# Optimization experiments

Measured on AMD Instinct MI355X. Metric: run time of the kernel, lower is better.

The kernel has to match this reference:

```python
import jax, jax.numpy as jnp
import numpy as np

R = 32          # voxel resolution
K = 3           # conv3d kernel size
GROUPS = 8      # GroupNorm groups
EPS_GN = 1e-5

def swish(x):
    return x * jax.nn.sigmoid(x)

def groupnorm(x, w, b):
    # x: (B, C, ...) -> normalize over (C//G, spatial) per group
    B, C = x.shape[0], x.shape[1]
    xs = x.reshape(B, GROUPS, C // GROUPS, -1)
    mu = xs.mean(axis=(2, 3), keepdims=True)
    var = xs.var(axis=(2, 3), keepdims=True)
    xs = (xs - mu) * jax.lax.rsqrt(var + EPS_GN)
    xs = xs.reshape(x.shape)
    shp = (1, C) + (1,) * (x.ndim - 2)
    return xs * w.reshape(shp) + b.reshape(shp)

def conv3d_same(x, w, b):
    y = jax.lax.conv_general_dilated(
        x, w, window_strides=(1, 1, 1), padding='SAME',
        dimension_numbers=('NCDHW', 'OIDHW', 'NCDHW'))
    return y + b[None, :, None, None, None]

def voxelize_coords(coords):
    # coords: (B,3,N) -> normalized coords in [0, R-1]
    nc = coords - coords.mean(axis=2, keepdims=True)
    scale = jnp.max(jnp.linalg.norm(nc, axis=1, keepdims=True), axis=2, keepdims=True) * 2.0
    nc = nc / scale + 0.5
    nc = jnp.clip(nc * R, 0.0, R - 1)
    return nc

def avg_voxelize(features, vox_coords):
    # features: (B,C,N), vox_coords: (B,3,N) int32 in [0,R-1]
    B, C, N = features.shape
    r3 = R * R * R
    flat = (vox_coords[:, 0] * R + vox_coords[:, 1]) * R + vox_coords[:, 2]  # (B,N)
    seg = (flat + jnp.arange(B, dtype=jnp.int32)[:, None] * r3).reshape(-1)
    feats = features.transpose(0, 2, 1).reshape(B * N, C)
    sums = jax.ops.segment_sum(feats, seg, num_segments=B * r3)
    cnt = jax.ops.segment_sum(jnp.ones((B * N,), features.dtype), seg, num_segments=B * r3)
    avg = sums / jnp.maximum(cnt, 1.0)[:, None]
    return avg.reshape(B, r3, C).transpose(0, 2, 1).reshape(B, C, R, R, R)

def trilinear_devoxelize(grid, nc):
    # grid: (B,C,R,R,R), nc: (B,3,N) float in [0,R-1]
    B, C = grid.shape[0], grid.shape[1]
    N = nc.shape[2]
    f = jnp.floor(nc)
    c0 = jnp.clip(f.astype(jnp.int32), 0, R - 1)
    c1 = jnp.clip(c0 + 1, 0, R - 1)
    w1 = nc - f
    w0 = 1.0 - w1
    gflat = grid.reshape(B, C, R * R * R)
    out = jnp.zeros((B, C, N), grid.dtype)
    for dx in (0, 1):
        for dy in (0, 1):
            for dz in (0, 1):
                xi = c1[:, 0] if dx else c0[:, 0]
                yi = c1[:, 1] if dy else c0[:, 1]
                zi = c1[:, 2] if dz else c0[:, 2]
                wx = w1[:, 0] if dx else w0[:, 0]
                wy = w1[:, 1] if dy else w0[:, 1]
                wz = w1[:, 2] if dz else w0[:, 2]
                idx = (xi * R + yi) * R + zi            # (B,N)
                vals = jnp.take_along_axis(gflat, idx[:, None, :], axis=2)
                out = out + vals * (wx * wy * wz)[:, None, :]
    return out

def setup_inputs() -> dict:
    key = jax.random.key(0)
    ks = jax.random.split(key, 16)
    B, Cin, Cout, N = 8, 64, 64, 16384
    s3 = 1.0 / np.sqrt(Cin * K * K * K)
    s3b = 1.0 / np.sqrt(Cout * K * K * K)
    s1 = 1.0 / np.sqrt(Cin)
    return {
        'features': jax.random.normal(ks[0], (B, Cin, N), jnp.float32),
        'coords': jax.random.normal(ks[1], (B, 3, N), jnp.float32),
        'conv1_w': jax.random.uniform(ks[2], (Cout, Cin, K, K, K), jnp.float32, -s3, s3),
        'conv1_b': jax.random.uniform(ks[3], (Cout,), jnp.float32, -s3, s3),
        'gn1_w': jnp.ones((Cout,), jnp.float32),
        'gn1_b': jnp.zeros((Cout,), jnp.float32),
        'conv2_w': jax.random.uniform(ks[4], (Cout, Cout, K, K, K), jnp.float32, -s3b, s3b),
        'conv2_b': jax.random.uniform(ks[5], (Cout,), jnp.float32, -s3b, s3b),
        'gn2_w': jnp.ones((Cout,), jnp.float32),
        'gn2_b': jnp.zeros((Cout,), jnp.float32),
        'pf_w': jax.random.uniform(ks[6], (Cout, Cin), jnp.float32, -s1, s1),
        'pf_b': jax.random.uniform(ks[7], (Cout,), jnp.float32, -s1, s1),
        'pf_gn_w': jnp.ones((Cout,), jnp.float32),
        'pf_gn_b': jnp.zeros((Cout,), jnp.float32),
    }

def reference(features, coords, conv1_w, conv1_b, gn1_w, gn1_b,
              conv2_w, conv2_b, gn2_w, gn2_b, pf_w, pf_b, pf_gn_w, pf_gn_b):
    coords_d = jax.lax.stop_gradient(coords)
    nc = voxelize_coords(coords_d)                       # (B,3,N) in [0,R-1]
    vox = jnp.round(nc).astype(jnp.int32)
    grid = avg_voxelize(features, vox)                   # (B,C,R,R,R)
    # voxel conv stack (dropout = identity in eval)
    g = conv3d_same(grid, conv1_w, conv1_b)
    g = swish(groupnorm(g, gn1_w, gn1_b))
    g = conv3d_same(g, conv2_w, conv2_b)
    g = groupnorm(g, gn2_w, gn2_b)
    voxel_feats = trilinear_devoxelize(g, nc)            # (B,Cout,N)
    # point branch: 1x1 conv1d + GroupNorm + Swish
    p = jnp.einsum('oc,bcn->bon', pf_w, features) + pf_b[None, :, None]
    p = swish(groupnorm(p, pf_gn_w, pf_gn_b))
    return voxel_feats + p
```

## Files before the change

### kernel.cpp

```cpp
#include <hip/hip_runtime.h>
#include <hip/hip_bf16.h>
#include <stdint.h>

#define PB 8
#define PN 16384
#define PC 64
#define PR 32
#define PR3 32768
#define PRP 34

typedef __attribute__((ext_vector_type(8))) short bf16x8;
typedef __attribute__((ext_vector_type(16))) float f32x16;

__device__ __forceinline__ unsigned short f2bf(float f) {
  union { float f; unsigned u; } v; v.f = f;
  unsigned r = v.u + 0x7FFFu + ((v.u >> 16) & 1u);
  return (unsigned short)(r >> 16);
}

__global__ void coord_stats_kernel(const float* __restrict__ coords, float* __restrict__ ms) {
  int b = blockIdx.x, t = threadIdx.x;
  __shared__ float wsum[4][3];
  __shared__ float wmax[4];
  __shared__ float meanv[3];
  const float* c0 = coords + (size_t)b * 3 * PN;
  float s0 = 0.f, s1 = 0.f, s2 = 0.f;
  for (int n = t; n < PN; n += 256) {
    s0 += c0[n]; s1 += c0[PN + n]; s2 += c0[2 * PN + n];
  }
  for (int off = 32; off > 0; off >>= 1) {
    s0 += __shfl_down(s0, off); s1 += __shfl_down(s1, off); s2 += __shfl_down(s2, off);
  }
  if ((t & 63) == 0) { wsum[t >> 6][0] = s0; wsum[t >> 6][1] = s1; wsum[t >> 6][2] = s2; }
  __syncthreads();
  if (t == 0) {
    for (int d = 0; d < 3; ++d)
      meanv[d] = (wsum[0][d] + wsum[1][d] + wsum[2][d] + wsum[3][d]) * (1.0f / PN);
  }
  __syncthreads();
  float m0 = meanv[0], m1 = meanv[1], m2 = meanv[2];
  float mx = 0.f;
  for (int n = t; n < PN; n += 256) {
    float dx = c0[n] - m0, dy = c0[PN + n] - m1, dz = c0[2 * PN + n] - m2;
    mx = fmaxf(mx, dx * dx + dy * dy + dz * dz);
  }
  for (int off = 32; off > 0; off >>= 1) mx = fmaxf(mx, __shfl_down(mx, off));
  if ((t & 63) == 0) wmax[t >> 6] = mx;
  __syncthreads();
  if (t == 0) {
    float m = fmaxf(fmaxf(wmax[0], wmax[1]), fmaxf(wmax[2], wmax[3]));
    ms[b * 4 + 0] = meanv[0]; ms[b * 4 + 1] = meanv[1]; ms[b * 4 + 2] = meanv[2];
    ms[b * 4 + 3] = 2.0f * sqrtf(m);
  }
}

__global__ void nc_vox_kernel(const float* __restrict__ coords, const float* __restrict__ ms,
                              float* __restrict__ nc, int* __restrict__ vflat) {
  int i = blockIdx.x * 256 + threadIdx.x;
  if (i >= PB * PN) return;
  int b = i >> 14, n = i & (PN - 1);
  float sc = ms[b * 4 + 3];
  int vi[3];
  #pragma unroll
  for (int d = 0; d < 3; ++d) {
    float c = coords[((size_t)b * 3 + d) * PN + n];
    float q = (c - ms[b * 4 + d]) / sc + 0.5f;
    float v = fminf(fmaxf(q * 32.0f, 0.0f), 31.0f);
    nc[((size_t)b * 3 + d) * PN + n] = v;
    vi[d] = (int)rintf(v);
  }
  vflat[i] = (vi[0] * PR + vi[1]) * PR + vi[2];
}

__global__ void scatter_kernel(const float* __restrict__ feats, const int* __restrict__ vflat,
                               float* __restrict__ sums, float* __restrict__ cnts) {
  int b = blockIdx.y, p0 = blockIdx.x * 64, t = threadIdx.x;
  __shared__ float fl[64 * 65];
  for (int k = 0; k < 16; ++k) {
    int i = t + k * 256;
    int c = i >> 6, p = i & 63;
    fl[c * 65 + p] = feats[((size_t)b * PC + c) * PN + p0 + p];
  }
  __syncthreads();
  if (t < 64) atomicAdd(&cnts[b * PR3 + vflat[b * PN + p0 + t]], 1.0f);
  int cc = t & 63, pp = t >> 6;
  for (int i = 0; i < 16; ++i) {
    int p = pp * 16 + i;
    int v = vflat[b * PN + p0 + p];
    atomicAdd(&sums[((size_t)b * PR3 + v) * PC + cc], fl[cc * 65 + p]);
  }
}

__global__ void finalize_kernel(const float* __restrict__ sums, const float* __restrict__ cnts,
                                unsigned short* __restrict__ g0) {
  int idx = blockIdx.x * 256 + threadIdx.x;
  int co = idx & 7, v = (idx >> 3) & (PR3 - 1), b = idx >> 18;
  float cnt = cnts[b * PR3 + v];
  float inv = 1.0f / fmaxf(cnt, 1.0f);
  const float4* sp = (const float4*)(sums + ((size_t)(b * PR3 + v) * PC) + co * 8);
  float4 A = sp[0], B4 = sp[1];
  float vals[8] = {A.x, A.y, A.z, A.w, B4.x, B4.y, B4.z, B4.w};
  unsigned short h[8];
  #pragma unroll
  for (int k = 0; k < 8; ++k) h[k] = f2bf(vals[k] * inv);
  int z = v >> 10, y = (v >> 5) & 31, x = v & 31;
  size_t o = ((((size_t)b * PRP + (z + 1)) * PRP + (y + 1)) * PRP + (x + 1)) * PC + co * 8;
  uint4 pk;
  pk.x = h[0] | ((unsigned)h[1] << 16); pk.y = h[2] | ((unsigned)h[3] << 16);
  pk.z = h[4] | ((unsigned)h[5] << 16); pk.w = h[6] | ((unsigned)h[7] << 16);
  *(uint4*)(g0 + o) = pk;
}

__global__ void tconv_kernel(const float* __restrict__ w, unsigned short* __restrict__ wkt) {
  int idx = blockIdx.x * 256 + threadIdx.x;
  if (idx >= 27 * 64 * 64) return;
  int i = idx & 63, o = (idx >> 6) & 63, tap = idx >> 12;
  wkt[idx] = f2bf(w[(o * 64 + i) * 27 + tap]);
}
__global__ void tpf_kernel(const float* __restrict__ pw, float* __restrict__ wt) {
  int idx = blockIdx.x * 256 + threadIdx.x;
  if (idx >= 4096) return;
  int o = idx & 63, ci = idx >> 6;
  wt[ci * 64 + o] = pw[o * 64 + ci];
}

__global__ __launch_bounds__(256, 1) void conv3_kernel(
    const unsigned short* __restrict__ gin, const unsigned short* __restrict__ wkt,
    const float* __restrict__ bias, float* __restrict__ outp, float* __restrict__ stats) {
  extern __shared__ char smem[];
  const int t = threadIdx.x;
  const int tile = blockIdx.x, b = blockIdx.y;
  const int tz = tile >> 4, ty = (tile >> 2) & 3, tx = tile & 3;
  const int z0 = tz * 8, y0 = ty * 8, x0 = tx * 8;

  {
    const size_t gbase = (size_t)b * (PRP * PRP * PRP * PC);
    for (int it = 0; it < 32; ++it) {
      int q = t + it * 256;
      if (q < 8000) {
        int vl = q >> 3, cc = q & 7;
        int zz = vl / 100, rem = vl - zz * 100;
        int yy = rem / 10, xx = rem - yy * 10;
        size_t go = gbase + (((size_t)(z0 + zz) * PRP + (y0 + yy)) * PRP + (x0 + xx)) * PC + cc * 8;
        uint4 d = *(const uint4*)(gin + go);
        *(uint4*)(smem + (vl * 128 + ((cc ^ (vl & 7)) << 4))) = d;
      }
    }
  }
  {
    #pragma unroll
    for (int u = 0; u < 2; ++u) {
      int q = t * 2 + u;
      int o = q >> 3, cc = q & 7;
      uint4 d = ((const uint4*)wkt)[q];
      *(uint4*)(smem + 128000 + (o * 128 + ((cc ^ (o & 7)) << 4))) = d;
    }
  }
  __syncthreads();

  const int wv = t >> 6, l31 = t & 31, hi = (t >> 5) & 1;
  int vbase[4];
  #pragma unroll
  for (int m = 0; m < 4; ++m) {
    int vi = wv * 128 + m * 32 + l31;
    int z = vi >> 6, y = (vi >> 3) & 7, x = vi & 7;
    vbase[m] = z * 100 + y * 10 + x;
  }

  f32x16 acc[4][2];
  #pragma unroll
  for (int m = 0; m < 4; ++m)
    #pragma unroll
    for (int nb = 0; nb < 2; ++nb)
      #pragma unroll
      for (int r = 0; r < 16; ++r) acc[m][nb][r] = 0.0f;

  for (int tap = 0; tap < 27; ++tap) {
    if (tap + 1 < 27) {
      char* wb = smem + 128000 + (((tap + 1) & 1) * 8192);
      #pragma unroll
      for (int u = 0; u < 2; ++u) {
        int q = t * 2 + u;
        int o = q >> 3, cc = q & 7;
        uint4 d = ((const uint4*)wkt)[(tap + 1) * 512 + q];
        *(uint4*)(wb + (o * 128 + ((cc ^ (o & 7)) << 4))) = d;
      }
    }
    const char* wb = smem + 128000 + ((tap & 1) * 8192);
    int dz = tap / 9, r9 = tap - dz * 9;
    int dy = r9 / 3, dx = r9 - dy * 3;
    int toff = dz * 100 + dy * 10 + dx;
    #pragma unroll
    for (int kk = 0; kk < 4; ++kk) {
      bf16x8 afr[4], bfr[2];
      #pragma unroll
      for (int m = 0; m < 4; ++m) {
        int vl = vbase[m] + toff;
        afr[m] = *(const bf16x8*)(smem + (vl * 128 + (((kk * 2 + hi) ^ (vl & 7)) << 4)));
      }
      #pragma unroll
      for (int nb = 0; nb < 2; ++nb) {
        int o = nb * 32 + l31;
        bfr[nb] = *(const bf16x8*)(wb + (o * 128 + (((kk * 2 + hi) ^ (o & 7)) << 4)));
      }
      #pragma unroll
      for (int m = 0; m < 4; ++m)
        #pragma unroll
        for (int nb = 0; nb < 2; ++nb)
          acc[m][nb] = __builtin_amdgcn_mfma_f32_32x32x16_bf16(afr[m], bfr[nb], acc[m][nb], 0, 0, 0);
    }
    __syncthreads();
  }

  float sg[2] = {0.f, 0.f}, ssg[2] = {0.f, 0.f};
  #pragma unroll
  for (int nb = 0; nb < 2; ++nb) {
    int cn = nb * 32 + l31;
    float bv = bias[cn];
    #pragma unroll
    for (int m = 0; m < 4; ++m) {
      #pragma unroll
      for (int r = 0; r < 16; ++r) {
        int row = (r & 3) + 8 * (r >> 2) + 4 * hi;
        int vi = wv * 128 + m * 32 + row;
        int Z = z0 + (vi >> 6), Y = y0 + ((vi >> 3) & 7), X = x0 + (vi & 7);
        int vg = (Z * PR + Y) * PR + X;
        float val = acc[m][nb][r] + bv;
        outp[((size_t)b * PR3 + vg) * PC + cn] = val;
        sg[nb] += val; ssg[nb] += val * val;
      }
    }
  }
  #pragma unroll
  for (int nb = 0; nb < 2; ++nb) {
    sg[nb] += __shfl_down(sg[nb], 32);
    ssg[nb] += __shfl_down(ssg[nb], 32);
    #pragma unroll
    for (int off = 1; off <= 4; off <<= 1) {
      sg[nb] += __shfl_xor(sg[nb], off);
      ssg[nb] += __shfl_xor(ssg[nb], off);
    }
  }
  if (hi == 0 && (l31 & 7) == 0) {
    #pragma unroll
    for (int nb = 0; nb < 2; ++nb) {
      int g = (nb * 32 + l31) >> 3;
      atomicAdd(&stats[((size_t)b * 8 + g) * 2 + 0], sg[nb]);
      atomicAdd(&stats[((size_t)b * 8 + g) * 2 + 1], ssg[nb]);
    }
  }
}

__global__ void gn_swish_bf16_kernel(const float* __restrict__ raw, const float* __restrict__ st,
                                     const float* __restrict__ gw, const float* __restrict__ gb,
                                     unsigned short* __restrict__ g1) {
  int idx = blockIdx.x * 256 + threadIdx.x;
  int co = idx & 7, v = (idx >> 3) & (PR3 - 1), b = idx >> 18;
  const float invM = 1.0f / (8.0f * PR3);
  float s = st[(b * 8 + co) * 2], ssv = st[(b * 8 + co) * 2 + 1];
  float mu = s * invM, var = ssv * invM - mu * mu;
  float rstd = rsqrtf(var + 1e-5f);
  const float4* rp = (const float4*)(raw + ((size_t)(b * PR3 + v) * PC + co * 8));
  float4 A = rp[0], B4 = rp[1];
  float vals[8] = {A.x, A.y, A.z, A.w, B4.x, B4.y, B4.z, B4.w};
  unsigned short h[8];
  #pragma unroll
  for (int k = 0; k < 8; ++k) {
    int c = co * 8 + k;
    float y = (vals[k] - mu) * rstd * gw[c] + gb[c];
    float sw = y / (1.0f + expf(-y));
    h[k] = f2bf(sw);
  }
  int z = v >> 10, yy = (v >> 5) & 31, x = v & 31;
  size_t o = ((((size_t)b * PRP + (z + 1)) * PRP + (yy + 1)) * PRP + (x + 1)) * PC + co * 8;
  uint4 pk;
  pk.x = h[0] | ((unsigned)h[1] << 16); pk.y = h[2] | ((unsigned)h[3] << 16);
  pk.z = h[4] | ((unsigned)h[5] << 16); pk.w = h[6] | ((unsigned)h[7] << 16);
  *(uint4*)(g1 + o) = pk;
}

__global__ void gn_inplace_kernel(float* __restrict__ raw, const float* __restrict__ st,
                                  const float* __restrict__ gw, const float* __restrict__ gb) {
  int idx = blockIdx.x * 256 + threadIdx.x;
  int co = idx & 7, v = (idx >> 3) & (PR3 - 1), b = idx >> 18;
  const float invM = 1.0f / (8.0f * PR3);
  float s = st[(b * 8 + co) * 2], ssv = st[(b * 8 + co) * 2 + 1];
  float mu = s * invM, var = ssv * invM - mu * mu;
  float rstd = rsqrtf(var + 1e-5f);
  float4* rp = (float4*)(raw + ((size_t)(b * PR3 + v) * PC + co * 8));
  float4 A = rp[0], B4 = rp[1];
  float vals[8] = {A.x, A.y, A.z, A.w, B4.x, B4.y, B4.z, B4.w};
  #pragma unroll
  for (int k = 0; k < 8; ++k) {
    int c = co * 8 + k;
    vals[k] = (vals[k] - mu) * rstd * gw[c] + gb[c];
  }
  rp[0] = make_float4(vals[0], vals[1], vals[2], vals[3]);
  rp[1] = make_float4(vals[4], vals[5], vals[6], vals[7]);
}

__global__ void pf_kernel(const float* __restrict__ feats, const float* __restrict__ wt,
                          const float* __restrict__ pb, float* __restrict__ praw,
                          float* __restrict__ stats) {
  int b = blockIdx.y, n0 = blockIdx.x * 64, t = threadIdx.x;
  __shared__ float fl[64 * 65];
  __shared__ float wl[64 * 64];
  for (int k = 0; k < 16; ++k) {
    int i = t + k * 256;
    int c = i >> 6, p = i & 63;
    fl[c * 65 + p] = feats[((size_t)b * PC + c) * PN + n0 + p];
    wl[i] = wt[i];
  }
  __syncthreads();
  int n = t & 63, q = t >> 6;
  float acc[16];
  #pragma unroll
  for (int j = 0; j < 16; ++j) acc[j] = pb[q * 16 + j];
  for (int ci = 0; ci < 64; ++ci) {
    float v = fl[ci * 65 + n];
    #pragma unroll
    for (int j = 0; j < 16; ++j) acc[j] += v * wl[ci * 64 + q * 16 + j];
  }
  float s[2] = {0.f, 0.f}, ss[2] = {0.f, 0.f};
  #pragma unroll
  for (int j = 0; j < 16; ++j) {
    int o = q * 16 + j;
    praw[((size_t)b * PC + o) * PN + n0 + n] = acc[j];
    int h = j >> 3;
    s[h] += acc[j]; ss[h] += acc[j] * acc[j];
  }
  #pragma unroll
  for (int h = 0; h < 2; ++h) {
    for (int off = 32; off > 0; off >>= 1) {
      s[h] += __shfl_down(s[h], off);
      ss[h] += __shfl_down(ss[h], off);
    }
  }
  if (n == 0) {
    #pragma unroll
    for (int h = 0; h < 2; ++h) {
      atomicAdd(&stats[((size_t)b * 8 + 2 * q + h) * 2 + 0], s[h]);
      atomicAdd(&stats[((size_t)b * 8 + 2 * q + h) * 2 + 1], ss[h]);
    }
  }
}

__global__ void devox_kernel(const float* __restrict__ g2, const float* __restrict__ nc,
                             const float* __restrict__ praw, const float* __restrict__ stpf,
                             const float* __restrict__ pgw, const float* __restrict__ pgb,
                             float* __restrict__ out) {
  int b = blockIdx.y, n0 = blockIdx.x * 64, t = threadIdx.x;
  __shared__ float lt[64][65];
  int wv = t >> 6, c = t & 63;
  for (int i = 0; i < 16; ++i) {
    int p = wv * 16 + i, n = n0 + p;
    float fx = nc[((size_t)b * 3 + 0) * PN + n];
    float fy = nc[((size_t)b * 3 + 1) * PN + n];
    float fz = nc[((size_t)b * 3 + 2) * PN + n];
    float flx = floorf(fx), fly = floorf(fy), flz = floorf(fz);
    int x0 = (int)flx, y0 = (int)fly, z0 = (int)flz;
    int x1 = min(x0 + 1, 31), y1 = min(y0 + 1, 31), z1 = min(z0 + 1, 31);
    float wx1 = fx - flx, wy1 = fy - fly, wz1 = fz - flz;
    float wx0 = 1.f - wx1, wy0 = 1.f - wy1, wz0 = 1.f - wz1;
    const float* gb2 = g2 + (size_t)b * PR3 * PC + c;
    float a = 0.f;
    a += gb2[(size_t)((x0 * PR + y0) * PR + z0) * PC] * (wx0 * wy0 * wz0);
    a += gb2[(size_t)((x0 * PR + y0) * PR + z1) * PC] * (wx0 * wy0 * wz1);
    a += gb2[(size_t)((x0 * PR + y1) * PR + z0) * PC] * (wx0 * wy1 * wz0);
    a += gb2[(size_t)((x0 * PR + y1) * PR + z1) * PC] * (wx0 * wy1 * wz1);
    a += gb2[(size_t)((x1 * PR + y0) * PR + z0) * PC] * (wx1 * wy0 * wz0);
    a += gb2[(size_t)((x1 * PR + y0) * PR + z1) * PC] * (wx1 * wy0 * wz1);
    a += gb2[(size_t)((x1 * PR + y1) * PR + z0) * PC] * (wx1 * wy1 * wz0);
    a += gb2[(size_t)((x1 * PR + y1) * PR + z1) * PC] * (wx1 * wy1 * wz1);
    lt[p][c] = a;
  }
  __syncthreads();
  int n = t & 63, q = t >> 6;
  const float invM = 1.0f / (8.0f * PN);
  float mu[2], rs[2];
  #pragma unroll
  for (int h = 0; h < 2; ++h) {
    float s = stpf[((size_t)b * 8 + 2 * q + h) * 2];
    float ssv = stpf[((size_t)b * 8 + 2 * q + h) * 2 + 1];
    float m_ = s * invM;
    mu[h] = m_;
    rs[h] = rsqrtf(ssv * invM - m_ * m_ + 1e-5f);
  }
  #pragma unroll
  for (int j = 0; j < 16; ++j) {
    int cc = q * 16 + j, h = j >> 3;
    float p_ = praw[((size_t)b * PC + cc) * PN + n0 + n];
    float y = (p_ - mu[h]) * rs[h] * pgw[cc] + pgb[cc];
    float sw = y / (1.0f + expf(-y));
    out[((size_t)b * PC + cc) * PN + n0 + n] = lt[n][cc] + sw;
  }
}

extern "C" void kernel_launch(void* const* d_in, const int* in_sizes, int n_in,
                              void* d_out, int out_size, void* d_ws, size_t ws_size,
                              hipStream_t stream) {
  (void)in_sizes; (void)n_in; (void)out_size; (void)ws_size;
  const float* features = (const float*)d_in[0];
  const float* coords   = (const float*)d_in[1];
  const float* conv1_w  = (const float*)d_in[2];
  const float* conv1_b  = (const float*)d_in[3];
  const float* gn1_w    = (const float*)d_in[4];
  const float* gn1_b    = (const float*)d_in[5];
  const float* conv2_w  = (const float*)d_in[6];
  const float* conv2_b  = (const float*)d_in[7];
  const float* gn2_w    = (const float*)d_in[8];
  const float* gn2_b    = (const float*)d_in[9];
  const float* pf_w     = (const float*)d_in[10];
  const float* pf_b     = (const float*)d_in[11];
  const float* pf_gn_w  = (const float*)d_in[12];
  const float* pf_gn_b  = (const float*)d_in[13];
  float* out = (float*)d_out;

  char* ws = (char*)d_ws;
  size_t off = 0;
  auto alloc = [&](size_t bytes) { size_t r = (off + 255) & ~(size_t)255; off = r + bytes; return r; };

  const size_t sz_nc   = (size_t)PB * 3 * PN * 4;
  const size_t sz_ms   = 256;
  const size_t sz_vf   = (size_t)PB * PN * 4;
  const size_t sz_cnt  = (size_t)PB * PR3 * 4;
  const size_t sz_st   = (size_t)PB * 8 * 2 * 4;
  const size_t sz_raw  = (size_t)PB * PR3 * PC * 4;
  const size_t sz_gpad = (size_t)PB * PRP * PRP * PRP * PC * 2;
  const size_t sz_wkt  = (size_t)27 * 64 * 64 * 2;
  const size_t sz_pfw  = (size_t)64 * 64 * 4;

  float*          nc    = (float*)(ws + alloc(sz_nc));
  float*          ms    = (float*)(ws + alloc(sz_ms));
  int*            vflat = (int*)(ws + alloc(sz_vf));
  float*          cnts  = (float*)(ws + alloc(sz_cnt));
  float*          st1   = (float*)(ws + alloc(sz_st));
  float*          st2   = (float*)(ws + alloc(sz_st));
  float*          stpf  = (float*)(ws + alloc(sz_st));
  float*          graw  = (float*)(ws + alloc(sz_raw));
  unsigned short* g0    = (unsigned short*)(ws + alloc(sz_gpad));
  unsigned short* g1    = (unsigned short*)(ws + alloc(sz_gpad));
  unsigned short* wkt1  = (unsigned short*)(ws + alloc(sz_wkt));
  unsigned short* wkt2  = (unsigned short*)(ws + alloc(sz_wkt));
  float*          pfwt  = (float*)(ws + alloc(sz_pfw));
  float*          praw  = (float*)g0;

  hipMemsetAsync(cnts, 0, sz_cnt, stream);
  hipMemsetAsync(graw, 0, sz_raw, stream);
  hipMemsetAsync(g0, 0, sz_gpad, stream);
  hipMemsetAsync(g1, 0, sz_gpad, stream);
  hipMemsetAsync(st1, 0, sz_st, stream);
  hipMemsetAsync(st2, 0, sz_st, stream);
  hipMemsetAsync(stpf, 0, sz_st, stream);

  tconv_kernel<<<(27 * 4096 + 255) / 256, 256, 0, stream>>>(conv1_w, wkt1);
  tconv_kernel<<<(27 * 4096 + 255) / 256, 256, 0, stream>>>(conv2_w, wkt2);
  tpf_kernel<<<16, 256, 0, stream>>>(pf_w, pfwt);

  coord_stats_kernel<<<PB, 256, 0, stream>>>(coords, ms);
  nc_vox_kernel<<<(PB * PN) / 256, 256, 0, stream>>>(coords, ms, nc, vflat);
  scatter_kernel<<<dim3(PN / 64, PB), 256, 0, stream>>>(features, vflat, graw, cnts);
  finalize_kernel<<<(PB * PR3 * 8) / 256, 256, 0, stream>>>(graw, cnts, g0);

  const size_t conv_lds = 128000 + 2 * 8192;
  conv3_kernel<<<dim3(64, PB), 256, conv_lds, stream>>>(g0, wkt1, conv1_b, graw, st1);
  gn_swish_bf16_kernel<<<(PB * PR3 * 8) / 256, 256, 0, stream>>>(graw, st1, gn1_w, gn1_b, g1);

  pf_kernel<<<dim3(PN / 64, PB), 256, 0, stream>>>(features, pfwt, pf_b, praw, stpf);

  conv3_kernel<<<dim3(64, PB), 256, conv_lds, stream>>>(g1, wkt2, conv2_b, graw, st2);
  gn_inplace_kernel<<<(PB * PR3 * 8) / 256, 256, 0, stream>>>(graw, st2, gn2_w, gn2_b);

  devox_kernel<<<dim3(PN / 64, PB), 256, 0, stream>>>(graw, nc, praw, stpf, pf_gn_w, pf_gn_b, out);
}
```

Baseline: 713.5 us.

## Fold second GroupNorm into devoxelize, zero only pad borders, register-tile pf

Removes the standalone in-place GroupNorm pass over the conv2 output. Instead, devox_kernel applies the per-channel scale and shift after trilinear interpolation, which is valid because the interpolation weights always sum to one. The full-buffer memsets of the padded bf16 grids are replaced by a kernel that zeroes only the border voxels, since the interior is overwritten anyway. The point-feature 1x1 conv is re-tiled so each thread computes a 4x4 block of outputs using float4 LDS loads and float4 stores, with a wave-level reduction for the statistics. Together these cut a large read/write pass over global memory and some memset traffic.

```diff
diff --git a/kernel.cpp b/kernel.cpp
--- a/kernel.cpp
+++ b/kernel.cpp
@@ -8,6 +8,7 @@
 #define PR 32
 #define PR3 32768
 #define PRP 34
+#define PRP3 (PRP * PRP * PRP)
 
 typedef __attribute__((ext_vector_type(8))) short bf16x8;
 typedef __attribute__((ext_vector_type(16))) float f32x16;
@@ -16,6 +17,16 @@
   union { float f; unsigned u; } v; v.f = f;
   unsigned r = v.u + 0x7FFFu + ((v.u >> 16) & 1u);
   return (unsigned short)(r >> 16);
+}
+
+__global__ void zero_pad_kernel(unsigned short* __restrict__ g) {
+  int idx = blockIdx.x * 256 + threadIdx.x;
+  if (idx >= PB * PRP3 * 8) return;
+  int v = (idx >> 3) % PRP3;
+  int z = v / (PRP * PRP), rem = v % (PRP * PRP), y = rem / PRP, x = rem % PRP;
+  bool border = (z == 0) | (z == PRP - 1) | (y == 0) | (y == PRP - 1) | (x == 0) | (x == PRP - 1);
+  if (!border) return;
+  *(uint4*)(g + ((size_t)idx << 3)) = make_uint4(0, 0, 0, 0);
 }
 
 __global__ void coord_stats_kernel(const float* __restrict__ coords, float* __restrict__ ms) {
@@ -279,79 +290,72 @@
   *(uint4*)(g1 + o) = pk;
 }
 
-__global__ void gn_inplace_kernel(float* __restrict__ raw, const float* __restrict__ st,
-                                  const float* __restrict__ gw, const float* __restrict__ gb) {
-  int idx = blockIdx.x * 256 + threadIdx.x;
-  int co = idx & 7, v = (idx >> 3) & (PR3 - 1), b = idx >> 18;
-  const float invM = 1.0f / (8.0f * PR3);
-  float s = st[(b * 8 + co) * 2], ssv = st[(b * 8 + co) * 2 + 1];
-  float mu = s * invM, var = ssv * invM - mu * mu;
-  float rstd = rsqrtf(var + 1e-5f);
-  float4* rp = (float4*)(raw + ((size_t)(b * PR3 + v) * PC + co * 8));
-  float4 A = rp[0], B4 = rp[1];
-  float vals[8] = {A.x, A.y, A.z, A.w, B4.x, B4.y, B4.z, B4.w};
-  #pragma unroll
-  for (int k = 0; k < 8; ++k) {
-    int c = co * 8 + k;
-    vals[k] = (vals[k] - mu) * rstd * gw[c] + gb[c];
-  }
-  rp[0] = make_float4(vals[0], vals[1], vals[2], vals[3]);
-  rp[1] = make_float4(vals[4], vals[5], vals[6], vals[7]);
-}
-
 __global__ void pf_kernel(const float* __restrict__ feats, const float* __restrict__ wt,
                           const float* __restrict__ pb, float* __restrict__ praw,
                           float* __restrict__ stats) {
   int b = blockIdx.y, n0 = blockIdx.x * 64, t = threadIdx.x;
-  __shared__ float fl[64 * 65];
+  __shared__ float fl[64 * 68];
   __shared__ float wl[64 * 64];
   for (int k = 0; k < 16; ++k) {
     int i = t + k * 256;
     int c = i >> 6, p = i & 63;
-    fl[c * 65 + p] = feats[((size_t)b * PC + c) * PN + n0 + p];
+    fl[c * 68 + p] = feats[((size_t)b * PC + c) * PN + n0 + p];
     wl[i] = wt[i];
   }
   __syncthreads();
-  int n = t & 63, q = t >> 6;
-  float acc[16];
-  #pragma unroll
-  for (int j = 0; j < 16; ++j) acc[j] = pb[q * 16 + j];
+  int po = (t & 15) * 4;
+  int oo = (t >> 4) * 4;
+  float acc[4][4];
+  #pragma unroll
+  for (int pi = 0; pi < 4; ++pi)
+    #pragma unroll
+    for (int oi = 0; oi < 4; ++oi) acc[pi][oi] = pb[oo + oi];
   for (int ci = 0; ci < 64; ++ci) {
-    float v = fl[ci * 65 + n];
-    #pragma unroll
-    for (int j = 0; j < 16; ++j) acc[j] += v * wl[ci * 64 + q * 16 + j];
-  }
-  float s[2] = {0.f, 0.f}, ss[2] = {0.f, 0.f};
-  #pragma unroll
-  for (int j = 0; j < 16; ++j) {
-    int o = q * 16 + j;
-    praw[((size_t)b * PC + o) * PN + n0 + n] = acc[j];
-    int h = j >> 3;
-    s[h] += acc[j]; ss[h] += acc[j] * acc[j];
-  }
-  #pragma unroll
-  for (int h = 0; h < 2; ++h) {
-    for (int off = 32; off > 0; off >>= 1) {
-      s[h] += __shfl_down(s[h], off);
-      ss[h] += __shfl_down(ss[h], off);
-    }
-  }
-  if (n == 0) {
-    #pragma unroll
-    for (int h = 0; h < 2; ++h) {
-      atomicAdd(&stats[((size_t)b * 8 + 2 * q + h) * 2 + 0], s[h]);
-      atomicAdd(&stats[((size_t)b * 8 + 2 * q + h) * 2 + 1], ss[h]);
-    }
-  }
-}
-
-__global__ void devox_kernel(const float* __restrict__ g2, const float* __restrict__ nc,
+    float4 fv = *(const float4*)(fl + ci * 68 + po);
+    float4 wv = *(const float4*)(wl + ci * 64 + oo);
+    float fa[4] = {fv.x, fv.y, fv.z, fv.w};
+    float wa[4] = {wv.x, wv.y, wv.z, wv.w};
+    #pragma unroll
+    for (int pi = 0; pi < 4; ++pi)
+      #pragma unroll
+      for (int oi = 0; oi < 4; ++oi) acc[pi][oi] += fa[pi] * wa[oi];
+  }
+  #pragma unroll
+  for (int oi = 0; oi < 4; ++oi) {
+    float4 st4 = make_float4(acc[0][oi], acc[1][oi], acc[2][oi], acc[3][oi]);
+    *(float4*)(praw + ((size_t)b * PC + oo + oi) * PN + n0 + po) = st4;
+  }
+  float s = 0.f, ss = 0.f;
+  #pragma unroll
+  for (int pi = 0; pi < 4; ++pi)
+    #pragma unroll
+    for (int oi = 0; oi < 4; ++oi) { float v = acc[pi][oi]; s += v; ss += v * v; }
+  #pragma unroll
+  for (int off = 1; off <= 16; off <<= 1) {
+    s += __shfl_xor(s, off); ss += __shfl_xor(ss, off);
+  }
+  if ((t & 31) == 0) {
+    int g = oo >> 3;
+    atomicAdd(&stats[((size_t)b * 8 + g) * 2 + 0], s);
+    atomicAdd(&stats[((size_t)b * 8 + g) * 2 + 1], ss);
+  }
+}
+
+__global__ void devox_kernel(const float* __restrict__ g2raw, const float* __restrict__ nc,
+                             const float* __restrict__ st2, const float* __restrict__ g2w,
+                             const float* __restrict__ g2b,
                              const float* __restrict__ praw, const float* __restrict__ stpf,
                              const float* __restrict__ pgw, const float* __restrict__ pgb,
                              float* __restrict__ out) {
   int b = blockIdx.y, n0 = blockIdx.x * 64, t = threadIdx.x;
   __shared__ float lt[64][65];
   int wv = t >> 6, c = t & 63;
+  const float invV = 1.0f / (8.0f * PR3);
+  float s2 = st2[(b * 8 + (c >> 3)) * 2], ss2 = st2[(b * 8 + (c >> 3)) * 2 + 1];
+  float mu2 = s2 * invV;
+  float rstd2 = rsqrtf(ss2 * invV - mu2 * mu2 + 1e-5f);
+  float sc = rstd2 * g2w[c];
+  float tc = g2b[c] - mu2 * sc;
   for (int i = 0; i < 16; ++i) {
     int p = wv * 16 + i, n = n0 + p;
     float fx = nc[((size_t)b * 3 + 0) * PN + n];
@@ -362,7 +366,7 @@
     int x1 = min(x0 + 1, 31), y1 = min(y0 + 1, 31), z1 = min(z0 + 1, 31);
     float wx1 = fx - flx, wy1 = fy - fly, wz1 = fz - flz;
     float wx0 = 1.f - wx1, wy0 = 1.f - wy1, wz0 = 1.f - wz1;
-    const float* gb2 = g2 + (size_t)b * PR3 * PC + c;
+    const float* gb2 = g2raw + (size_t)b * PR3 * PC + c;
     float a = 0.f;
     a += gb2[(size_t)((x0 * PR + y0) * PR + z0) * PC] * (wx0 * wy0 * wz0);
     a += gb2[(size_t)((x0 * PR + y0) * PR + z1) * PC] * (wx0 * wy0 * wz1);
@@ -372,7 +376,7 @@
     a += gb2[(size_t)((x1 * PR + y0) * PR + z1) * PC] * (wx1 * wy0 * wz1);
     a += gb2[(size_t)((x1 * PR + y1) * PR + z0) * PC] * (wx1 * wy1 * wz0);
     a += gb2[(size_t)((x1 * PR + y1) * PR + z1) * PC] * (wx1 * wy1 * wz1);
-    lt[p][c] = a;
+    lt[p][c] = a * sc + tc;
   }
   __syncthreads();
   int n = t & 63, q = t >> 6;
@@ -426,7 +430,7 @@
   const size_t sz_cnt  = (size_t)PB * PR3 * 4;
   const size_t sz_st   = (size_t)PB * 8 * 2 * 4;
   const size_t sz_raw  = (size_t)PB * PR3 * PC * 4;
-  const size_t sz_gpad = (size_t)PB * PRP * PRP * PRP * PC * 2;
+  const size_t sz_gpad = (size_t)PB * PRP3 * PC * 2;
   const size_t sz_wkt  = (size_t)27 * 64 * 64 * 2;
   const size_t sz_pfw  = (size_t)64 * 64 * 4;
 
@@ -447,11 +451,13 @@
 
   hipMemsetAsync(cnts, 0, sz_cnt, stream);
   hipMemsetAsync(graw, 0, sz_raw, stream);
-  hipMemsetAsync(g0, 0, sz_gpad, stream);
-  hipMemsetAsync(g1, 0, sz_gpad, stream);
   hipMemsetAsync(st1, 0, sz_st, stream);
   hipMemsetAsync(st2, 0, sz_st, stream);
   hipMemsetAsync(stpf, 0, sz_st, stream);
+
+  const int zp_blocks = (PB * PRP3 * 8 + 255) / 256;
+  zero_pad_kernel<<<zp_blocks, 256, 0, stream>>>(g0);
+  zero_pad_kernel<<<zp_blocks, 256, 0, stream>>>(g1);
 
   tconv_kernel<<<(27 * 4096 + 255) / 256, 256, 0, stream>>>(conv1_w, wkt1);
   tconv_kernel<<<(27 * 4096 + 255) / 256, 256, 0, stream>>>(conv2_w, wkt2);
@@ -469,7 +475,7 @@
   pf_kernel<<<dim3(PN / 64, PB), 256, 0, stream>>>(features, pfwt, pf_b, praw, stpf);
 
   conv3_kernel<<<dim3(64, PB), 256, conv_lds, stream>>>(g1, wkt2, conv2_b, graw, st2);
-  gn_inplace_kernel<<<(PB * PR3 * 8) / 256, 256, 0, stream>>>(graw, st2, gn2_w, gn2_b);
-
-  devox_kernel<<<dim3(PN / 64, PB), 256, 0, stream>>>(graw, nc, praw, stpf, pf_gn_w, pf_gn_b, out);
-}
+
+  devox_kernel<<<dim3(PN / 64, PB), 256, 0, stream>>>(graw, nc, st2, gn2_w, gn2_b,
+                                                      praw, stpf, pf_gn_w, pf_gn_b, out);
+}
```

New measurement: 615.6 us. 1.16x faster.
